# Optimization experiments

Hardware: AMD Instinct MI355X
Metric: run time of the kernel (lower is better)

The kernel has to match this reference:

```python
import jax, jax.numpy as jnp
import numpy as np

B, L, D = 4, 4096, 2048
E = 64           # num_experts
K = 2            # top_k
AUX_W = 0.01     # aux_loss_weight


def setup_inputs() -> dict:
    key = jax.random.key(0)
    kx, kw = jax.random.split(key)
    x = jax.random.normal(kx, (B, L, D), dtype=jnp.float32)
    W = jax.random.normal(kw, (E, D), dtype=jnp.float32) * 0.02  # nn.init.normal_(std=0.02)
    return {"x": x, "W": W}


def reference(x, W):
    # gate: logits [B, L, E]
    logits = jnp.einsum('bld,ed->ble', x, W)
    # full softmax over experts (used for aux loss)
    probs = jax.nn.softmax(logits, axis=-1)
    # top-k selection and renormalized weights
    top_k_logits, top_k_indices = jax.lax.top_k(logits, K)      # [B, L, K]
    top_k_weights = jax.nn.softmax(top_k_logits, axis=-1)       # [B, L, K]
    # load-balance aux loss (Switch-style): uses top-1 expert assignment
    expert_mask = jax.nn.one_hot(top_k_indices[..., 0], E, dtype=jnp.float32)  # [B, L, E]
    expert_fraction = expert_mask.mean(axis=(0, 1))              # [E]
    prob_fraction = probs.mean(axis=(0, 1))                      # [E]
    aux_loss = E * jnp.sum(expert_fraction * prob_fraction) * AUX_W
    return top_k_indices, top_k_weights, aux_loss
```

## Files before the change

### kernel.cpp

```cpp
#include <hip/hip_runtime.h>

typedef float f32x16 __attribute__((ext_vector_type(16)));

#define D_DIM 2048
#define E_NUM 64
#define M_TOK 16384
#define BK 32
#define XS_ROW 36
#define XS_TILE (64 * XS_ROW)


__global__ __launch_bounds__(256) void wg_kernel(const float* __restrict__ W,
                                                 float* __restrict__ Wg,
                                                 float* __restrict__ g) {
    if (blockIdx.x == 0 && threadIdx.x < 128) g[threadIdx.x] = 0.0f;
    const int i4 = blockIdx.x * 256 + threadIdx.x;
    const int e  = i4 >> 9;
    const int k4 = (i4 & 511) << 2;
    const float4 v = *(const float4*)&W[e * D_DIM + k4];
    const int base = (((k4 >> 10) << 3) + (e >> 3)) * 8192 + (k4 & 1023) * 8 + (e & 7);
    Wg[base + 0]  = v.x;
    Wg[base + 8]  = v.y;
    Wg[base + 16] = v.z;
    Wg[base + 24] = v.w;
}

__global__ __launch_bounds__(1024) void fused_kernel(
    const float* __restrict__ x, const float* __restrict__ Wg,
    float* __restrict__ out, float* __restrict__ gprob, float* __restrict__ gcnt)
{
    __shared__ float lds[4 * XS_TILE];

    const int tid  = threadIdx.x;
    const int wid  = tid >> 6;
    const int lane = tid & 63;
    const int h    = wid >> 3;
    const int eb   = (wid & 7) << 3;
    const long tok0 = (long)blockIdx.x * 64;
    const int wslab = __builtin_amdgcn_readfirstlane(((h << 3) + (wid & 7)) * 8192);

    const int sh   = tid >> 9;
    const int ss   = tid & 511;
    const int srow = ss >> 3;
    const int sc   = (ss & 7) << 2;
    const float* xsrc = x + (tok0 + srow) * D_DIM + (sh << 10) + sc;

    double accd[8];
    #pragma unroll
    for (int e = 0; e < 8; ++e) accd[e] = 0.0;

    float4 v0 = *(const float4*)(xsrc);
    *(float4*)&lds[(sh * 2) * XS_TILE + srow * XS_ROW + sc] = v0;
    __syncthreads();

    for (int it = 0; it < 32; ++it) {
        if (it < 31) v0 = *(const float4*)(xsrc + (it + 1) * BK);
        const float* xb = lds + (h * 2 + (it & 1)) * XS_TILE + lane * XS_ROW;
        #pragma unroll 1
        for (int c2 = 0; c2 < 2; ++c2) {
            float accc[8];
            #pragma unroll
            for (int e = 0; e < 8; ++e) accc[e] = 0.0f;
            const float* xc = xb + c2 * 16;
            const f32x16* wp = (const f32x16*)(Wg + wslab + it * 256 + c2 * 128);
            #pragma unroll 1
            for (int hc = 0; hc < 2; ++hc) {
                const f32x16 wA = wp[hc * 4 + 0];
                const f32x16 wB = wp[hc * 4 + 1];
                const f32x16 wC = wp[hc * 4 + 2];
                const f32x16 wD = wp[hc * 4 + 3];
                const float4 xa = *(const float4*)(xc + hc * 8);
                const float4 xb4 = *(const float4*)(xc + hc * 8 + 4);
                #pragma unroll
                for (int e = 0; e < 8; ++e) {
                    float a = accc[e];
                    a += xa.x  * wA[e];
                    a += xa.y  * wA[8 + e];
                    a += xa.z  * wB[e];
                    a += xa.w  * wB[8 + e];
                    a += xb4.x * wC[e];
                    a += xb4.y * wC[8 + e];
                    a += xb4.z * wD[e];
                    a += xb4.w * wD[8 + e];
                    accc[e] = a;
                }
            }
            #pragma unroll
            for (int e = 0; e < 8; ++e) accd[e] += (double)accc[e];
        }
        if (it < 31)
            *(float4*)&lds[(sh * 2 + ((it + 1) & 1)) * XS_TILE + srow * XS_ROW + sc] = v0;
        __syncthreads();
    }

    {
        float* sp = lds + h * 4096 + lane * 64 + eb;
        *(float4*)(sp + 0) = make_float4((float)accd[0], (float)accd[1],
                                         (float)accd[2], (float)accd[3]);
        *(float4*)(sp + 4) = make_float4((float)accd[4], (float)accd[5],
                                         (float)accd[6], (float)accd[7]);
    }
    __syncthreads();

    float pacc = 0.0f, cacc = 0.0f;
    if (wid < 4) {
        const int q = wid;
        for (int i = 0; i < 16; ++i) {
            const int  tl = q * 16 + i;
            const long t  = tok0 + tl;
            const float l = lds[tl * 64 + lane] + lds[4096 + tl * 64 + lane];
            float m1 = l; int i1 = lane;
            #pragma unroll
            for (int off = 32; off > 0; off >>= 1) {
                const float ov = __shfl_xor(m1, off, 64);
                const int   oi = __shfl_xor(i1, off, 64);
                if (ov > m1 || (ov == m1 && oi < i1)) { m1 = ov; i1 = oi; }
            }
            const float p = __expf(l - m1);
            float s = p;
            #pragma unroll
            for (int off = 32; off > 0; off >>= 1) s += __shfl_xor(s, off, 64);
            pacc += p / s;
            if (lane == i1) cacc += 1.0f;
            const float lm = (lane == i1) ? -1e30f : l;
            float m2 = lm; int i2 = lane;
            #pragma unroll
            for (int off = 32; off > 0; off >>= 1) {
                const float ov = __shfl_xor(m2, off, 64);
                const int   oi = __shfl_xor(i2, off, 64);
                if (ov > m2 || (ov == m2 && oi < i2)) { m2 = ov; i2 = oi; }
            }
            if (lane == 0) {
                out[2 * t]     = (float)i1;
                out[2 * t + 1] = (float)i2;
                const float w1 = 1.0f / (1.0f + __expf(m2 - m1));
                out[2 * M_TOK + 2 * t]     = w1;
                out[2 * M_TOK + 2 * t + 1] = 1.0f - w1;
            }
        }
    }
    __syncthreads();
    if (wid < 4) {
        lds[wid * 64 + lane]       = pacc;
        lds[256 + wid * 64 + lane] = cacc;
    }
    __syncthreads();
    if (wid == 0) {
        atomicAdd(&gprob[lane], lds[lane] + lds[64 + lane] + lds[128 + lane] + lds[192 + lane]);
        atomicAdd(&gcnt[lane],  lds[256 + lane] + lds[320 + lane] + lds[384 + lane] + lds[448 + lane]);
    }
}

__global__ __launch_bounds__(64) void aux_kernel(
    const float* __restrict__ gprob, const float* __restrict__ gcnt,
    float* __restrict__ out)
{
    const int lane = threadIdx.x;
    float v = gprob[lane] * gcnt[lane];
    #pragma unroll
    for (int off = 32; off > 0; off >>= 1) v += __shfl_xor(v, off, 64);
    if (lane == 0)
        out[4 * M_TOK] = 64.0f * 0.01f * v / ((float)M_TOK * (float)M_TOK);
}

extern "C" void kernel_launch(void* const* d_in, const int* in_sizes, int n_in,
                              void* d_out, int out_size, void* d_ws, size_t ws_size,
                              hipStream_t stream)
{
    const float* x = (const float*)d_in[0];
    const float* W = (const float*)d_in[1];
    float* out   = (float*)d_out;
    float* gprob = (float*)d_ws;
    float* gcnt  = gprob + 64;
    float* Wg    = gprob + 128;

    wg_kernel<<<128, 256, 0, stream>>>(W, Wg, gprob);
    fused_kernel<<<256, 1024, 0, stream>>>(x, Wg, out, gprob, gcnt);
    aux_kernel<<<1, 64, 0, stream>>>(gprob, gcnt, out);
}
```

Before: 259.6 us.

## Software-prefetch W slabs one step ahead and transpose W via LDS

The inner dot-product loop now splits into four steps of four k-values. Each step loads the next step's pair of 16-float W vectors while computing with the current pair, so global/L2 load latency overlaps the FMAs and fewer W registers are live at once. The W re-layout kernel now stages through shared memory, giving coalesced float4 reads and writes from 16 blocks instead of 128 blocks doing scattered scalar stores. The cost is more loop iterations with a smaller per-iteration body, plus a clamped redundant load on the final step.

After: 287.7 us. 1.11x slower.

```diff
diff --git a/kernel.cpp b/kernel.cpp
--- a/kernel.cpp
+++ b/kernel.cpp
@@ -13,16 +13,30 @@
 __global__ __launch_bounds__(256) void wg_kernel(const float* __restrict__ W,
                                                  float* __restrict__ Wg,
                                                  float* __restrict__ g) {
-    if (blockIdx.x == 0 && threadIdx.x < 128) g[threadIdx.x] = 0.0f;
-    const int i4 = blockIdx.x * 256 + threadIdx.x;
-    const int e  = i4 >> 9;
-    const int k4 = (i4 & 511) << 2;
-    const float4 v = *(const float4*)&W[e * D_DIM + k4];
-    const int base = (((k4 >> 10) << 3) + (e >> 3)) * 8192 + (k4 & 1023) * 8 + (e & 7);
-    Wg[base + 0]  = v.x;
-    Wg[base + 8]  = v.y;
-    Wg[base + 16] = v.z;
-    Wg[base + 24] = v.w;
+    __shared__ float t[8][1025];
+    const int b  = blockIdx.x;
+    const int h  = b >> 3, gq = b & 7;
+    const int tid = threadIdx.x;
+    if (b == 0 && tid < 128) g[tid] = 0.0f;
+    #pragma unroll
+    for (int p = 0; p < 8; ++p) {
+        const int e  = tid >> 5;
+        const int k4 = ((tid & 31) << 2) + p * 128;
+        const float4 v = *(const float4*)&W[(size_t)(gq * 8 + e) * D_DIM + h * 1024 + k4];
+        t[e][k4 + 0] = v.x; t[e][k4 + 1] = v.y;
+        t[e][k4 + 2] = v.z; t[e][k4 + 3] = v.w;
+    }
+    __syncthreads();
+    float* dst = Wg + (size_t)b * 8192;
+    #pragma unroll
+    for (int p = 0; p < 8; ++p) {
+        const int off = p * 1024 + tid * 4;
+        const int kk = off >> 3, e0 = off & 7;
+        float4 v;
+        v.x = t[e0 + 0][kk]; v.y = t[e0 + 1][kk];
+        v.z = t[e0 + 2][kk]; v.w = t[e0 + 3][kk];
+        *(float4*)&dst[off] = v;
+    }
 }
 
 __global__ __launch_bounds__(1024) void fused_kernel(
@@ -38,6 +52,7 @@
     const int eb   = (wid & 7) << 3;
     const long tok0 = (long)blockIdx.x * 64;
     const int wslab = __builtin_amdgcn_readfirstlane(((h << 3) + (wid & 7)) * 8192);
+    const f32x16* wq = (const f32x16*)(Wg + wslab);
 
     const int sh   = tid >> 9;
     const int ss   = tid & 511;
@@ -51,6 +66,8 @@
 
     float4 v0 = *(const float4*)(xsrc);
     *(float4*)&lds[(sh * 2) * XS_TILE + srow * XS_ROW + sc] = v0;
+    f32x16 wc0 = wq[0];
+    f32x16 wc1 = wq[1];
     __syncthreads();
 
     for (int it = 0; it < 32; ++it) {
@@ -62,28 +79,23 @@
             #pragma unroll
             for (int e = 0; e < 8; ++e) accc[e] = 0.0f;
             const float* xc = xb + c2 * 16;
-            const f32x16* wp = (const f32x16*)(Wg + wslab + it * 256 + c2 * 128);
+            const int sb0 = it * 8 + c2 * 4;
             #pragma unroll 1
-            for (int hc = 0; hc < 2; ++hc) {
-                const f32x16 wA = wp[hc * 4 + 0];
-                const f32x16 wB = wp[hc * 4 + 1];
-                const f32x16 wC = wp[hc * 4 + 2];
-                const f32x16 wD = wp[hc * 4 + 3];
-                const float4 xa = *(const float4*)(xc + hc * 8);
-                const float4 xb4 = *(const float4*)(xc + hc * 8 + 4);
+            for (int s = 0; s < 4; ++s) {
+                const int nx = (sb0 + s + 1 < 256) ? (sb0 + s + 1) : 255;
+                const f32x16 wn0 = wq[nx * 2];
+                const f32x16 wn1 = wq[nx * 2 + 1];
+                const float4 xa = *(const float4*)(xc + s * 4);
                 #pragma unroll
                 for (int e = 0; e < 8; ++e) {
                     float a = accc[e];
-                    a += xa.x  * wA[e];
-                    a += xa.y  * wA[8 + e];
-                    a += xa.z  * wB[e];
-                    a += xa.w  * wB[8 + e];
-                    a += xb4.x * wC[e];
-                    a += xb4.y * wC[8 + e];
-                    a += xb4.z * wD[e];
-                    a += xb4.w * wD[8 + e];
+                    a += xa.x * wc0[e];
+                    a += xa.y * wc0[8 + e];
+                    a += xa.z * wc1[e];
+                    a += xa.w * wc1[8 + e];
                     accc[e] = a;
                 }
+                wc0 = wn0; wc1 = wn1;
             }
             #pragma unroll
             for (int e = 0; e < 8; ++e) accd[e] += (double)accc[e];
@@ -174,7 +186,7 @@
     float* gcnt  = gprob + 64;
     float* Wg    = gprob + 128;
 
-    wg_kernel<<<128, 256, 0, stream>>>(W, Wg, gprob);
+    wg_kernel<<<16, 256, 0, stream>>>(W, Wg, gprob);
     fused_kernel<<<256, 1024, 0, stream>>>(x, Wg, out, gprob, gcnt);
     aux_kernel<<<1, 64, 0, stream>>>(gprob, gcnt, out);
 }
```
